# Optimization experiments

Hardware: AMD Instinct MI355X
Metric: run time of the kernel (lower is better)

Reference implementation:

```python
import jax, jax.numpy as jnp
import numpy as np

N, E, D, L = 50000, 625000, 128, 7
EPS = 1e-7   # GENConv message epsilon
T = 1.0      # softmax aggregation temperature (learn_t=False)
NUM_ATOM_FEATS, ATOM_VOCAB = 9, 64
NUM_BOND_FEATS, BOND_VOCAB = 3, 8


def setup_inputs() -> dict:
    key = jax.random.key(0)
    ks = jax.random.split(key, 9)
    x = jax.random.randint(ks[0], (N, NUM_ATOM_FEATS), 0, ATOM_VOCAB, dtype=jnp.int32)
    edge_index = jax.random.randint(ks[1], (2, E), 0, N, dtype=jnp.int32)
    edge_attr = jax.random.randint(ks[2], (E, NUM_BOND_FEATS), 0, BOND_VOCAB, dtype=jnp.int32)
    atom_emb = jax.random.normal(ks[3], (NUM_ATOM_FEATS, ATOM_VOCAB, D), dtype=jnp.float32) * 0.1
    bond_emb = jax.random.normal(ks[4], (NUM_BOND_FEATS, BOND_VOCAB, D), dtype=jnp.float32) * 0.1
    W = jax.random.normal(ks[5], (L, D, D), dtype=jnp.float32) / np.sqrt(D).astype(np.float32)
    b = jnp.zeros((L, D), dtype=jnp.float32)
    ln_gamma = jnp.ones((L, D), dtype=jnp.float32)
    ln_beta = jnp.zeros((L, D), dtype=jnp.float32)
    return dict(x=x, edge_index=edge_index, edge_attr=edge_attr,
                atom_emb=atom_emb, bond_emb=bond_emb, W=W, b=b,
                ln_gamma=ln_gamma, ln_beta=ln_beta)


def _layer_norm(h, g, bta):
    mu = jnp.mean(h, axis=-1, keepdims=True)
    var = jnp.var(h, axis=-1, keepdims=True)
    return (h - mu) * jax.lax.rsqrt(var + 1e-5) * g + bta


def _gen_conv(h, src, dst, edge_emb, Wl, bl):
    # GENConv: msg = relu(x_j + e) + eps; softmax aggregation over dst; Linear(x + m)
    msg = jax.nn.relu(h[src] + edge_emb) + EPS                 # [E, D]
    logits = msg * T
    seg_max = jax.ops.segment_max(logits, dst, num_segments=N)  # [N, D]
    seg_max = jnp.where(jnp.isfinite(seg_max), seg_max, 0.0)    # empty segments
    e = jnp.exp(logits - seg_max[dst])                          # [E, D]
    denom = jax.ops.segment_sum(e, dst, num_segments=N)         # [N, D]
    alpha = e / (denom[dst] + 1e-16)
    m = jax.ops.segment_sum(alpha * msg, dst, num_segments=N)   # [N, D]
    return (h + m) @ Wl + bl


def reference(x, edge_index, edge_attr, atom_emb, bond_emb, W, b, ln_gamma, ln_beta):
    src, dst = edge_index[0], edge_index[1]
    # AtomEncoder: sum of per-feature embedding lookups -> [N, D]
    h = jnp.sum(atom_emb[jnp.arange(NUM_ATOM_FEATS)[None, :], x], axis=1)
    # BondEncoder (conv_encode_edge=False: encoded once) -> [E, D]
    edge_emb = jnp.sum(bond_emb[jnp.arange(NUM_BOND_FEATS)[None, :], edge_attr], axis=1)
    # res+ block, dropout=0 (no-op)
    h = _gen_conv(h, src, dst, edge_emb, W[0], b[0])
    for layer in range(1, L):
        h2 = jax.nn.relu(_layer_norm(h, ln_gamma[layer - 1], ln_beta[layer - 1]))
        h = _gen_conv(h2, src, dst, edge_emb, W[layer], b[layer]) + h
    h = _layer_norm(h, ln_gamma[L - 1], ln_beta[L - 1])
    return h
```

## Files before the change

### kernel.cpp

```cpp
#include <hip/hip_runtime.h>
#include <hip/hip_fp16.h>
#include <math.h>


constexpr int D = 128;
constexpr int NA = 9;
constexpr int NB = 3;
constexpr float L2E = 1.4426950408889634f;
constexpr float INV_L2E = 0.6931471805599453f;

using half8  = __attribute__((ext_vector_type(8))) _Float16;
using h2v    = __attribute__((ext_vector_type(2))) _Float16;
using floatx4 = __attribute__((ext_vector_type(4))) float;


__global__ void k_hist(const int* __restrict__ dst, int* __restrict__ deg, int E) {
    int e = blockIdx.x * 256 + threadIdx.x;
    if (e < E) atomicAdd(&deg[dst[e]], 1);
}

__global__ void k_scan_a(const int* __restrict__ deg, int* __restrict__ offs,
                         int* __restrict__ bsum, int N) {
    __shared__ int s[256];
    int i = blockIdx.x * 256 + threadIdx.x;
    int v = (i < N) ? deg[i] : 0;
    s[threadIdx.x] = v;
    __syncthreads();
    for (int d = 1; d < 256; d <<= 1) {
        int add = (threadIdx.x >= d) ? s[threadIdx.x - d] : 0;
        __syncthreads();
        s[threadIdx.x] += add;
        __syncthreads();
    }
    if (i < N) offs[i + 1] = s[threadIdx.x];
    if (threadIdx.x == 255) bsum[blockIdx.x] = s[255];
    if (i == 0) offs[0] = 0;
}

__global__ void k_scan_b(const int* __restrict__ bsum, int* __restrict__ bexc, int nb) {
    __shared__ int s[256];
    int t = threadIdx.x;
    int v = (t < nb) ? bsum[t] : 0;
    s[t] = v;
    __syncthreads();
    for (int d = 1; d < 256; d <<= 1) {
        int add = (t >= d) ? s[t - d] : 0;
        __syncthreads();
        s[t] += add;
        __syncthreads();
    }
    if (t < nb) bexc[t] = s[t] - v;
}

__global__ void k_scan_c_dhist(int* __restrict__ offs, const int* __restrict__ bexc,
                               const int* __restrict__ deg, int* __restrict__ dbin,
                               int N) {
    __shared__ int lb[64];
    int t = threadIdx.x;
    if (t < 64) lb[t] = 0;
    __syncthreads();
    int i = blockIdx.x * 256 + t;
    if (i < N) {
        offs[i + 1] += bexc[blockIdx.x];
        int d = deg[i]; d = d < 63 ? d : 63;
        atomicAdd(&lb[63 - d], 1);
    }
    __syncthreads();
    if (t < 64 && lb[t] > 0) atomicAdd(&dbin[t], lb[t]);
}

__global__ void k_fill(const int* __restrict__ src, const int* __restrict__ dst,
                       const int* __restrict__ attr, const int* __restrict__ offs,
                       int* __restrict__ cur, unsigned* __restrict__ recs1,
                       const int* __restrict__ dbin, int* __restrict__ doff, int E) {
    int e = blockIdx.x * 256 + threadIdx.x;
    if (e < E) {
        int d = dst[e];
        int pos = offs[d] + atomicAdd(&cur[d], 1);
        unsigned cidx = (unsigned)(attr[e * 3] * 64 + attr[e * 3 + 1] * 8 + attr[e * 3 + 2]);
        recs1[pos] = (unsigned)src[e] | (cidx << 17);
    }
    if (blockIdx.x == 0 && threadIdx.x == 0) {
        int acc = 0;
        for (int b = 0; b < 64; ++b) { doff[b] = acc; acc += dbin[b]; }
    }
}


__global__ void k_dfill(const int* __restrict__ deg, const int* __restrict__ doff,
                        int* __restrict__ dcur, const int* __restrict__ offs,
                        int4* __restrict__ meta, int N) {
    __shared__ int lc[64], lbase[64];
    int t = threadIdx.x;
    if (t < 64) lc[t] = 0;
    __syncthreads();
    int i = blockIdx.x * 256 + t;
    int b = 0, rank = 0;
    if (i < N) {
        int d = deg[i]; d = d < 63 ? d : 63;
        b = 63 - d;
        rank = atomicAdd(&lc[b], 1);
    }
    __syncthreads();
    if (t < 64 && lc[t] > 0) lbase[t] = atomicAdd(&dcur[t], lc[t]);
    __syncthreads();
    if (i < N)
        meta[doff[b] + lbase[b] + rank] = make_int4(offs[i], offs[i + 1], i, 0);
}

__global__ void k_comb(const float* __restrict__ bemb, __half* __restrict__ comb16,
                       int* __restrict__ deg, int* __restrict__ cur,
                       int* __restrict__ dbin, int* __restrict__ dcur,
                       int4* __restrict__ meta, int N, int N4) {
    int gid = blockIdx.x * 256 + threadIdx.x;
    if (gid < N) { deg[gid] = 0; cur[gid] = 0; }
    if (gid < 64) { dbin[gid] = 0; dcur[gid] = 0; }
    if (gid >= N && gid < N4) meta[gid] = make_int4(0, 0, -1, 0);
    if (gid >= 512 * 32) return;
    int c = gid >> 5, q = gid & 31;
    int a0 = c >> 6, a1 = (c >> 3) & 7, a2 = c & 7;
    float4 v0 = *(const float4*)(bemb + (a0)*D + q * 4);
    float4 v1 = *(const float4*)(bemb + (8 + a1) * D + q * 4);
    float4 v2 = *(const float4*)(bemb + (16 + a2) * D + q * 4);
    __half2* c2 = (__half2*)comb16;
    c2[c * 64 + q * 2]     = __floats2half2_rn(L2E * (v0.x + v1.x + v2.x),
                                               L2E * (v0.y + v1.y + v2.y));
    c2[c * 64 + q * 2 + 1] = __floats2half2_rn(L2E * (v0.z + v1.z + v2.z),
                                               L2E * (v0.w + v1.w + v2.w));
}

__global__ void k_wt(const float* __restrict__ W, __half* __restrict__ Wt16, int total) {
    int o = blockIdx.x * 256 + threadIdx.x;
    if (o >= total) return;
    int l = o >> 14;
    int rem = o & 16383;
    int f = rem >> 7, k = rem & 127;
    Wt16[o] = __float2half_rn(W[(l << 14) + k * 128 + f]);
}


__global__ void k_atom(const int* __restrict__ x, const float* __restrict__ aemb,
                       __half* __restrict__ h16, int N) {
    int wid = (blockIdx.x * blockDim.x + threadIdx.x) >> 6;
    int lane = threadIdx.x & 63;
    if (wid >= N) return;
    const int* xr = x + wid * NA;
    float ax = 0.f, ay = 0.f;
#pragma unroll
    for (int f = 0; f < NA; ++f) {
        int v = xr[f];
        const float2 e = *(const float2*)(aemb + (f * 64 + v) * D + 2 * lane);
        ax += e.x; ay += e.y;
    }
    ((__half2*)h16)[wid * 64 + lane] = __floats2half2_rn(ax * L2E, ay * L2E);
}


__global__ __launch_bounds__(256) void k_agg(const __half* __restrict__ h16,
                      const unsigned* __restrict__ recs1,
                      const int4* __restrict__ meta,
                      const __half* __restrict__ comb16,
                      __half* __restrict__ t16, int N) {
    int w = (blockIdx.x * blockDim.x + threadIdx.x) >> 6;
    int lane = threadIdx.x & 63;
    int base = w * 4;
    if (base >= N) return;

    const h2v* hrow = (const h2v*)h16 + lane;
    const h2v* crow = (const h2v*)comb16 + lane;
    const h2v zero2 = (h2v)(_Float16)0;

    int4 m0 = meta[base], m1 = meta[base + 1], m2 = meta[base + 2], m3 = meta[base + 3];
    int su0 = __builtin_amdgcn_readfirstlane(m0.x), eu0 = __builtin_amdgcn_readfirstlane(m0.y), nid0 = __builtin_amdgcn_readfirstlane(m0.z);
    int su1 = __builtin_amdgcn_readfirstlane(m1.x), eu1 = __builtin_amdgcn_readfirstlane(m1.y), nid1 = __builtin_amdgcn_readfirstlane(m1.z);
    int su2 = __builtin_amdgcn_readfirstlane(m2.x), eu2 = __builtin_amdgcn_readfirstlane(m2.y), nid2 = __builtin_amdgcn_readfirstlane(m2.z);
    int su3 = __builtin_amdgcn_readfirstlane(m3.x), eu3 = __builtin_amdgcn_readfirstlane(m3.y), nid3 = __builtin_amdgcn_readfirstlane(m3.z);

    unsigned rv0 = 0, rv1 = 0, rv2 = 0, rv3 = 0;
    if (su0 < eu0) { int ri = su0 + lane; ri = (ri < eu0 - 1) ? ri : eu0 - 1; rv0 = recs1[ri]; }
    if (su1 < eu1) { int ri = su1 + lane; ri = (ri < eu1 - 1) ? ri : eu1 - 1; rv1 = recs1[ri]; }
    if (su2 < eu2) { int ri = su2 + lane; ri = (ri < eu2 - 1) ? ri : eu2 - 1; rv2 = recs1[ri]; }
    if (su3 < eu3) { int ri = su3 + lane; ri = (ri < eu3 - 1) ? ri : eu3 - 1; rv3 = recs1[ri]; }

    auto process = [&](int su, int eu, int nid, unsigned recv) {
        if (nid < 0) return;
        h2v hm2 = hrow[nid * 64];
        if (su >= eu) {
            ((__half2*)t16)[nid * 64 + lane] = __floats2half2_rn(
                (float)hm2[0] * INV_L2E, (float)hm2[1] * INV_L2E);
            return;
        }
        float Sx = 0.f, Sy = 0.f, Wx = 0.f, Wy = 0.f;
        h2v hq[16], cq[16];
        int e0 = su;
        bool first = true;
        do {
            int lastc = (eu < e0 + 64) ? eu : e0 + 64;
            int last = lastc - 1;
            if (!first) {
                int ri = e0 + lane;
                ri = (ri < eu - 1) ? ri : eu - 1;
                recv = recs1[ri];
            }
            first = false;

            auto load4 = [&](int b2, int slot) {
#pragma unroll
                for (int i = 0; i < 4; ++i) {
                    int idx = b2 + i; idx = (idx < last) ? idx : last;
                    unsigned r = __builtin_amdgcn_readlane(recv, idx - e0);
                    int sj = (int)(r & 0x1FFFFu);
                    int cj = (int)(r >> 17);
                    hq[slot * 4 + i] = hrow[sj * 64];
                    cq[slot * 4 + i] = crow[cj * 64];
                }
            };
            auto comp4u = [&](int slot) {
#pragma unroll
                for (int i = 0; i < 4; ++i) {
                    h2v m = hq[slot * 4 + i] + cq[slot * 4 + i];
                    m = __builtin_elementwise_max(m, zero2);
                    float u0 = (float)m[0], u1 = (float)m[1];
                    float px = __builtin_amdgcn_exp2f(u0);
                    float py = __builtin_amdgcn_exp2f(u1);
                    Sx += px; Sy += py;
                    Wx = fmaf(px, u0, Wx);
                    Wy = fmaf(py, u1, Wy);
                }
            };
            auto comp4m = [&](int gb, int slot) {
#pragma unroll
                for (int i = 0; i < 4; ++i) {
                    h2v m = hq[slot * 4 + i] + cq[slot * 4 + i];
                    m = __builtin_elementwise_max(m, zero2);
                    float u0 = (float)m[0], u1 = (float)m[1];
                    bool valid = (gb + i) < eu;
                    float px = valid ? __builtin_amdgcn_exp2f(u0) : 0.f;
                    float py = valid ? __builtin_amdgcn_exp2f(u1) : 0.f;
                    Sx += px; Sy += py;
                    Wx = fmaf(px, u0, Wx);
                    Wy = fmaf(py, u1, Wy);
                }
            };

            load4(e0, 0);
            if (e0 + 4  < lastc) load4(e0 + 4, 1);
            if (e0 + 8  < lastc) load4(e0 + 8, 2);
            if (e0 + 12 < lastc) load4(e0 + 12, 3);

            int e = e0;
            for (; e + 16 < lastc; e += 16) {
                comp4u(0); load4(e + 16, 0);
                comp4u(1); load4(e + 20, 1);
                comp4u(2); load4(e + 24, 2);
                comp4u(3); load4(e + 28, 3);
            }
            comp4m(e, 0);
            if (e + 4  < lastc) comp4m(e + 4, 1);
            if (e + 8  < lastc) comp4m(e + 8, 2);
            if (e + 12 < lastc) comp4m(e + 12, 3);

            e0 = lastc;
        } while (e0 < eu);

        float tx = ((float)hm2[0] + Wx / (Sx + 1e-16f)) * INV_L2E;
        float ty = ((float)hm2[1] + Wy / (Sy + 1e-16f)) * INV_L2E;
        ((__half2*)t16)[nid * 64 + lane] = __floats2half2_rn(tx, ty);
    };

    process(su0, eu0, nid0, rv0);
    process(su1, eu1, nid1, rv1);
    process(su2, eu2, nid2, rv2);
    process(su3, eu3, nid3, rv3);
}


template <int MODE>
__global__ __launch_bounds__(256) void k_gemm(const __half* __restrict__ A16,
                                              const __half* __restrict__ Wt16,
                                              const float* __restrict__ bl,
                                              const __half* __restrict__ res16,
                                              __half* __restrict__ hres16,
                                              const float* __restrict__ g,
                                              const float* __restrict__ bta,
                                              __half* __restrict__ h16,
                                              float* __restrict__ out,
                                              int N, int useRes) {
    __shared__ float2 sm[2][2][16];
    int lane = threadIdx.x & 63;
    int wave = threadIdx.x >> 6;
    int grp = wave >> 1, half = wave & 1;
    int quad = lane >> 4, col = lane & 15;
    int node = blockIdx.x * 32 + grp * 16 + col;
    bool nok = node < N;
    int nc = nok ? node : N - 1;

    const __half* arow = A16 + (size_t)nc * 128;
    half8 bfrag[4];
#pragma unroll
    for (int ks = 0; ks < 4; ++ks)
        bfrag[ks] = *(const half8*)(arow + ks * 32 + quad * 8);

    uint2 rr[4];
    if (useRes) {
#pragma unroll
        for (int ft2 = 0; ft2 < 4; ++ft2) {
            int f0 = (half * 4 + ft2) * 16 + quad * 4;
            rr[ft2] = *(const uint2*)(res16 + (size_t)nc * 128 + f0);
        }
    }

    floatx4 acc[4];
#pragma unroll
    for (int ft2 = 0; ft2 < 4; ++ft2) acc[ft2] = (floatx4){0.f, 0.f, 0.f, 0.f};

#pragma unroll
    for (int ft2 = 0; ft2 < 4; ++ft2) {
        const __half* wrow = Wt16 + (size_t)((half * 4 + ft2) * 16 + col) * 128;
#pragma unroll
        for (int ks = 0; ks < 4; ++ks) {
            half8 afrag = *(const half8*)(wrow + ks * 32 + quad * 8);
            acc[ft2] = __builtin_amdgcn_mfma_f32_16x16x32_f16(afrag, bfrag[ks],
                                                              acc[ft2], 0, 0, 0);
        }
    }

    float s = 0.f, ss = 0.f;
#pragma unroll
    for (int ft2 = 0; ft2 < 4; ++ft2) {
        int f0 = (half * 4 + ft2) * 16 + quad * 4;
        float4 bb = *(const float4*)(bl + f0);
        float o0 = acc[ft2][0] + bb.x, o1 = acc[ft2][1] + bb.y;
        float o2 = acc[ft2][2] + bb.z, o3 = acc[ft2][3] + bb.w;
        if (useRes) {
            __half2 r01 = *(__half2*)&rr[ft2].x, r23 = *(__half2*)&rr[ft2].y;
            o0 += __low2float(r01); o1 += __high2float(r01);
            o2 += __low2float(r23); o3 += __high2float(r23);
        }
        acc[ft2][0] = o0; acc[ft2][1] = o1; acc[ft2][2] = o2; acc[ft2][3] = o3;
        s += (o0 + o1) + (o2 + o3);
        ss += fmaf(o0, o0, o1 * o1) + fmaf(o2, o2, o3 * o3);
        if (MODE == 0 && nok) {
            __half2 h01 = __floats2half2_rn(o0, o1);
            __half2 h23 = __floats2half2_rn(o2, o3);
            uint2 pk = make_uint2(*(unsigned*)&h01, *(unsigned*)&h23);
            *(uint2*)(hres16 + (size_t)node * 128 + f0) = pk;
        }
    }
    s += __shfl_xor(s, 16, 64);  ss += __shfl_xor(ss, 16, 64);
    s += __shfl_xor(s, 32, 64);  ss += __shfl_xor(ss, 32, 64);
    if (quad == 0) sm[grp][half][col] = make_float2(s, ss);
    __syncthreads();
    float2 oth = sm[grp][half ^ 1][col];
    float st = s + oth.x, sst = ss + oth.y;
    float mu = st * (1.f / 128.f);
    float var = sst * (1.f / 128.f) - mu * mu;
    float rs = rsqrtf(var + 1e-5f);

#pragma unroll
    for (int ft2 = 0; ft2 < 4; ++ft2) {
        int f0 = (half * 4 + ft2) * 16 + quad * 4;
        float4 gg = *(const float4*)(g + f0);
        float4 bt = *(const float4*)(bta + f0);
        float l0 = (acc[ft2][0] - mu) * rs * gg.x + bt.x;
        float l1 = (acc[ft2][1] - mu) * rs * gg.y + bt.y;
        float l2 = (acc[ft2][2] - mu) * rs * gg.z + bt.z;
        float l3 = (acc[ft2][3] - mu) * rs * gg.w + bt.w;
        if (MODE == 0) {
            l0 = fmaxf(l0, 0.f); l1 = fmaxf(l1, 0.f);
            l2 = fmaxf(l2, 0.f); l3 = fmaxf(l3, 0.f);
            if (nok) {
                __half2 h01 = __floats2half2_rn(l0 * L2E, l1 * L2E);
                __half2 h23 = __floats2half2_rn(l2 * L2E, l3 * L2E);
                uint2 pk = make_uint2(*(unsigned*)&h01, *(unsigned*)&h23);
                *(uint2*)(h16 + (size_t)node * 128 + f0) = pk;
            }
        } else {
            if (nok)
                *(float4*)(out + (size_t)node * 128 + f0) =
                    make_float4(l0, l1, l2, l3);
        }
    }
}


extern "C" void kernel_launch(void* const* d_in, const int* in_sizes, int n_in,
                              void* d_out, int out_size, void* d_ws, size_t ws_size,
                              hipStream_t stream) {
    const int*   x    = (const int*)d_in[0];
    const int*   ei   = (const int*)d_in[1];
    const int*   attr = (const int*)d_in[2];
    const float* aemb = (const float*)d_in[3];
    const float* bemb = (const float*)d_in[4];
    const float* Wf   = (const float*)d_in[5];
    const float* bf   = (const float*)d_in[6];
    const float* gam  = (const float*)d_in[7];
    const float* bet  = (const float*)d_in[8];
    float* out = (float*)d_out;

    const int N = in_sizes[0] / NA;
    const int E = in_sizes[1] / 2;
    const int L = in_sizes[5] / (D * D);
    const int N4 = (N + 3) & ~3;

    char* ws = (char*)d_ws;
    size_t o = 0;
    auto carve = [&](size_t bytes) -> void* {
        void* p = (void*)(ws + o);
        o += (bytes + 255) & ~(size_t)255;
        return p;
    };
    __half* hres16 = (__half*)carve((size_t)N * D * 2);
    __half* h16    = (__half*)carve((size_t)N * D * 2);
    __half* t16    = (__half*)carve((size_t)N * D * 2);
    unsigned* recs1 = (unsigned*)carve((size_t)E * 4);
    __half* comb16 = (__half*)carve(512 * D * 2);
    __half* Wt16   = (__half*)carve((size_t)L * D * D * 2);
    int*    deg    = (int*)carve((size_t)N * 4);
    int*    cur    = (int*)carve((size_t)N * 4);
    int*    offs   = (int*)carve((size_t)(N + 1) * 4);
    int4*   meta   = (int4*)carve((size_t)N4 * 16);
    int*    dbin   = (int*)carve(256);
    int*    doff   = (int*)carve(256);
    int*    dcur   = (int*)carve(256);
    int*    bsum   = (int*)carve(4096);
    int*    bexc   = (int*)carve(4096);

    const int* src = ei;
    const int* dst = ei + E;

    int ebl = (E + 255) / 256;
    int nbl = (N + 255) / 256;

    k_comb<<<nbl, 256, 0, stream>>>(bemb, comb16, deg, cur, dbin, dcur, meta, N, N4);
    int wtot = L * D * D;
    k_wt<<<(wtot + 255) / 256, 256, 0, stream>>>(Wf, Wt16, wtot);
    k_hist<<<ebl, 256, 0, stream>>>(dst, deg, E);
    k_scan_a<<<nbl, 256, 0, stream>>>(deg, offs, bsum, N);
    k_scan_b<<<1, 256, 0, stream>>>(bsum, bexc, nbl);
    k_scan_c_dhist<<<nbl, 256, 0, stream>>>(offs, bexc, deg, dbin, N);
    k_fill<<<ebl, 256, 0, stream>>>(src, dst, attr, offs, cur, recs1, dbin, doff, E);
    k_dfill<<<nbl, 256, 0, stream>>>(deg, doff, dcur, offs, meta, N);

    int wbl = (N * 64 + 255) / 256;
    k_atom<<<wbl, 256, 0, stream>>>(x, aemb, h16, N);

    int nwv = N4 / 4;
    int abl = (nwv * 64 + 255) / 256;
    int gbl = (N + 31) / 32;
    for (int l = 0; l < L; ++l) {
        k_agg<<<abl, 256, 0, stream>>>(h16, recs1, meta, comb16, t16, N);
        if (l == L - 1) {
            k_gemm<1><<<gbl, 256, 0, stream>>>(t16, Wt16 + l * D * D, bf + l * D,
                                               hres16, hres16,
                                               gam + l * D, bet + l * D, h16, out,
                                               N, 1);
        } else {
            k_gemm<0><<<gbl, 256, 0, stream>>>(t16, Wt16 + l * D * D, bf + l * D,
                                               hres16, hres16,
                                               gam + l * D, bet + l * D, h16, out,
                                               N, l > 0 ? 1 : 0);
        }
    }
}
```

Measured before the change: 590.2 us.

## Fuse setup kernels, drop cursor array, pad edge records to remove clamps

Merges the bond-combination, weight-transpose and zeroing kernels into one setup kernel, and merges the degree-bucket fill with the atom encoder, cutting the launch count. The fill step now advances the offsets array in place with atomics, which removes the separate cursor array. Start and end offsets are then read from the shifted offsets. The edge record buffer is padded with 64 zeroed entries so the aggregation kernel can drop index clamping when it loads records. Chunks shrink from 64 to 48 edges, likely so that readlane indices stay within the wavefront after the clamp is removed.

```diff
diff --git a/kernel.cpp b/kernel.cpp
--- a/kernel.cpp
+++ b/kernel.cpp
@@ -12,6 +12,37 @@
 using half8  = __attribute__((ext_vector_type(8))) _Float16;
 using h2v    = __attribute__((ext_vector_type(2))) _Float16;
 using floatx4 = __attribute__((ext_vector_type(4))) float;
+
+
+__global__ void k_setup0(const float* __restrict__ bemb, __half* __restrict__ comb16,
+                         const float* __restrict__ W, __half* __restrict__ Wt16,
+                         int* __restrict__ deg, int* __restrict__ dbin,
+                         int* __restrict__ dcur, int4* __restrict__ meta,
+                         unsigned* __restrict__ recs1,
+                         int N, int N4, int wtot, int E) {
+    int gid = blockIdx.x * 256 + threadIdx.x;
+    if (gid < N) deg[gid] = 0;
+    if (gid < 64) { dbin[gid] = 0; dcur[gid] = 0; recs1[E + gid] = 0; }
+    if (gid >= N && gid < N4) meta[gid] = make_int4(0, 0, -1, 0);
+    if (gid < 512 * 32) {
+        int c = gid >> 5, q = gid & 31;
+        int a0 = c >> 6, a1 = (c >> 3) & 7, a2 = c & 7;
+        float4 v0 = *(const float4*)(bemb + (a0)*D + q * 4);
+        float4 v1 = *(const float4*)(bemb + (8 + a1) * D + q * 4);
+        float4 v2 = *(const float4*)(bemb + (16 + a2) * D + q * 4);
+        __half2* c2 = (__half2*)comb16;
+        c2[c * 64 + q * 2]     = __floats2half2_rn(L2E * (v0.x + v1.x + v2.x),
+                                                   L2E * (v0.y + v1.y + v2.y));
+        c2[c * 64 + q * 2 + 1] = __floats2half2_rn(L2E * (v0.z + v1.z + v2.z),
+                                                   L2E * (v0.w + v1.w + v2.w));
+    }
+    if (gid < wtot) {
+        int l = gid >> 14;
+        int rem = gid & 16383;
+        int f = rem >> 7, k = rem & 127;
+        Wt16[gid] = __float2half_rn(W[(l << 14) + k * 128 + f]);
+    }
+}
 
 
 __global__ void k_hist(const int* __restrict__ dst, int* __restrict__ deg, int E) {
@@ -70,13 +101,13 @@
 }
 
 __global__ void k_fill(const int* __restrict__ src, const int* __restrict__ dst,
-                       const int* __restrict__ attr, const int* __restrict__ offs,
-                       int* __restrict__ cur, unsigned* __restrict__ recs1,
+                       const int* __restrict__ attr, int* __restrict__ offs,
+                       unsigned* __restrict__ recs1,
                        const int* __restrict__ dbin, int* __restrict__ doff, int E) {
     int e = blockIdx.x * 256 + threadIdx.x;
     if (e < E) {
         int d = dst[e];
-        int pos = offs[d] + atomicAdd(&cur[d], 1);
+        int pos = atomicAdd(&offs[d], 1);
         unsigned cidx = (unsigned)(attr[e * 3] * 64 + attr[e * 3 + 1] * 8 + attr[e * 3 + 2]);
         recs1[pos] = (unsigned)src[e] | (cidx << 17);
     }
@@ -87,60 +118,32 @@
 }
 
 
-__global__ void k_dfill(const int* __restrict__ deg, const int* __restrict__ doff,
-                        int* __restrict__ dcur, const int* __restrict__ offs,
-                        int4* __restrict__ meta, int N) {
-    __shared__ int lc[64], lbase[64];
-    int t = threadIdx.x;
-    if (t < 64) lc[t] = 0;
-    __syncthreads();
-    int i = blockIdx.x * 256 + t;
-    int b = 0, rank = 0;
-    if (i < N) {
-        int d = deg[i]; d = d < 63 ? d : 63;
-        b = 63 - d;
-        rank = atomicAdd(&lc[b], 1);
-    }
-    __syncthreads();
-    if (t < 64 && lc[t] > 0) lbase[t] = atomicAdd(&dcur[t], lc[t]);
-    __syncthreads();
-    if (i < N)
-        meta[doff[b] + lbase[b] + rank] = make_int4(offs[i], offs[i + 1], i, 0);
-}
-
-__global__ void k_comb(const float* __restrict__ bemb, __half* __restrict__ comb16,
-                       int* __restrict__ deg, int* __restrict__ cur,
-                       int* __restrict__ dbin, int* __restrict__ dcur,
-                       int4* __restrict__ meta, int N, int N4) {
-    int gid = blockIdx.x * 256 + threadIdx.x;
-    if (gid < N) { deg[gid] = 0; cur[gid] = 0; }
-    if (gid < 64) { dbin[gid] = 0; dcur[gid] = 0; }
-    if (gid >= N && gid < N4) meta[gid] = make_int4(0, 0, -1, 0);
-    if (gid >= 512 * 32) return;
-    int c = gid >> 5, q = gid & 31;
-    int a0 = c >> 6, a1 = (c >> 3) & 7, a2 = c & 7;
-    float4 v0 = *(const float4*)(bemb + (a0)*D + q * 4);
-    float4 v1 = *(const float4*)(bemb + (8 + a1) * D + q * 4);
-    float4 v2 = *(const float4*)(bemb + (16 + a2) * D + q * 4);
-    __half2* c2 = (__half2*)comb16;
-    c2[c * 64 + q * 2]     = __floats2half2_rn(L2E * (v0.x + v1.x + v2.x),
-                                               L2E * (v0.y + v1.y + v2.y));
-    c2[c * 64 + q * 2 + 1] = __floats2half2_rn(L2E * (v0.z + v1.z + v2.z),
-                                               L2E * (v0.w + v1.w + v2.w));
-}
-
-__global__ void k_wt(const float* __restrict__ W, __half* __restrict__ Wt16, int total) {
-    int o = blockIdx.x * 256 + threadIdx.x;
-    if (o >= total) return;
-    int l = o >> 14;
-    int rem = o & 16383;
-    int f = rem >> 7, k = rem & 127;
-    Wt16[o] = __float2half_rn(W[(l << 14) + k * 128 + f]);
-}
-
-
-__global__ void k_atom(const int* __restrict__ x, const float* __restrict__ aemb,
-                       __half* __restrict__ h16, int N) {
+__global__ void k_dfill_atom(const int* __restrict__ deg, const int* __restrict__ doff,
+                             int* __restrict__ dcur, const int* __restrict__ offs,
+                             int4* __restrict__ meta,
+                             const int* __restrict__ x, const float* __restrict__ aemb,
+                             __half* __restrict__ h16, int N, int nbl) {
+    if ((int)blockIdx.x < nbl) {
+        __shared__ int lc[64], lbase[64];
+        int t = threadIdx.x;
+        if (t < 64) lc[t] = 0;
+        __syncthreads();
+        int i = blockIdx.x * 256 + t;
+        int b = 0, rank = 0;
+        if (i < N) {
+            int d = deg[i]; d = d < 63 ? d : 63;
+            b = 63 - d;
+            rank = atomicAdd(&lc[b], 1);
+        }
+        __syncthreads();
+        if (t < 64 && lc[t] > 0) lbase[t] = atomicAdd(&dcur[t], lc[t]);
+        __syncthreads();
+        if (i < N) {
+            int su = (i > 0) ? offs[i - 1] : 0;
+            int eu = offs[i];
+            meta[doff[b] + lbase[b] + rank] = make_int4(su, eu, i, 0);
+        }
+    }
     int wid = (blockIdx.x * blockDim.x + threadIdx.x) >> 6;
     int lane = threadIdx.x & 63;
     if (wid >= N) return;
@@ -177,10 +180,10 @@
     int su3 = __builtin_amdgcn_readfirstlane(m3.x), eu3 = __builtin_amdgcn_readfirstlane(m3.y), nid3 = __builtin_amdgcn_readfirstlane(m3.z);
 
     unsigned rv0 = 0, rv1 = 0, rv2 = 0, rv3 = 0;
-    if (su0 < eu0) { int ri = su0 + lane; ri = (ri < eu0 - 1) ? ri : eu0 - 1; rv0 = recs1[ri]; }
-    if (su1 < eu1) { int ri = su1 + lane; ri = (ri < eu1 - 1) ? ri : eu1 - 1; rv1 = recs1[ri]; }
-    if (su2 < eu2) { int ri = su2 + lane; ri = (ri < eu2 - 1) ? ri : eu2 - 1; rv2 = recs1[ri]; }
-    if (su3 < eu3) { int ri = su3 + lane; ri = (ri < eu3 - 1) ? ri : eu3 - 1; rv3 = recs1[ri]; }
+    if (su0 < eu0) rv0 = recs1[su0 + lane];
+    if (su1 < eu1) rv1 = recs1[su1 + lane];
+    if (su2 < eu2) rv2 = recs1[su2 + lane];
+    if (su3 < eu3) rv3 = recs1[su3 + lane];
 
     auto process = [&](int su, int eu, int nid, unsigned recv) {
         if (nid < 0) return;
@@ -193,22 +196,13 @@
         float Sx = 0.f, Sy = 0.f, Wx = 0.f, Wy = 0.f;
         h2v hq[16], cq[16];
         int e0 = su;
-        bool first = true;
-        do {
-            int lastc = (eu < e0 + 64) ? eu : e0 + 64;
-            int last = lastc - 1;
-            if (!first) {
-                int ri = e0 + lane;
-                ri = (ri < eu - 1) ? ri : eu - 1;
-                recv = recs1[ri];
-            }
-            first = false;
+        for (;;) {
+            int lastc = (eu < e0 + 48) ? eu : e0 + 48;
 
             auto load4 = [&](int b2, int slot) {
 #pragma unroll
                 for (int i = 0; i < 4; ++i) {
-                    int idx = b2 + i; idx = (idx < last) ? idx : last;
-                    unsigned r = __builtin_amdgcn_readlane(recv, idx - e0);
+                    unsigned r = __builtin_amdgcn_readlane(recv, b2 + i - e0);
                     int sj = (int)(r & 0x1FFFFu);
                     int cj = (int)(r >> 17);
                     hq[slot * 4 + i] = hrow[sj * 64];
@@ -234,7 +228,7 @@
                     h2v m = hq[slot * 4 + i] + cq[slot * 4 + i];
                     m = __builtin_elementwise_max(m, zero2);
                     float u0 = (float)m[0], u1 = (float)m[1];
-                    bool valid = (gb + i) < eu;
+                    bool valid = (gb + i) < lastc;
                     float px = valid ? __builtin_amdgcn_exp2f(u0) : 0.f;
                     float py = valid ? __builtin_amdgcn_exp2f(u1) : 0.f;
                     Sx += px; Sy += py;
@@ -261,7 +255,9 @@
             if (e + 12 < lastc) comp4m(e + 12, 3);
 
             e0 = lastc;
-        } while (e0 < eu);
+            if (e0 >= eu) break;
+            recv = recs1[e0 + lane];
+        }
 
         float tx = ((float)hm2[0] + Wx / (Sx + 1e-16f)) * INV_L2E;
         float ty = ((float)hm2[1] + Wy / (Sy + 1e-16f)) * INV_L2E;
@@ -413,11 +409,10 @@
     __half* hres16 = (__half*)carve((size_t)N * D * 2);
     __half* h16    = (__half*)carve((size_t)N * D * 2);
     __half* t16    = (__half*)carve((size_t)N * D * 2);
-    unsigned* recs1 = (unsigned*)carve((size_t)E * 4);
+    unsigned* recs1 = (unsigned*)carve((size_t)(E + 64) * 4);
     __half* comb16 = (__half*)carve(512 * D * 2);
     __half* Wt16   = (__half*)carve((size_t)L * D * D * 2);
     int*    deg    = (int*)carve((size_t)N * 4);
-    int*    cur    = (int*)carve((size_t)N * 4);
     int*    offs   = (int*)carve((size_t)(N + 1) * 4);
     int4*   meta   = (int4*)carve((size_t)N4 * 16);
     int*    dbin   = (int*)carve(256);
@@ -431,19 +426,21 @@
 
     int ebl = (E + 255) / 256;
     int nbl = (N + 255) / 256;
-
-    k_comb<<<nbl, 256, 0, stream>>>(bemb, comb16, deg, cur, dbin, dcur, meta, N, N4);
     int wtot = L * D * D;
-    k_wt<<<(wtot + 255) / 256, 256, 0, stream>>>(Wf, Wt16, wtot);
+    int s0max = wtot > N4 ? wtot : N4;
+    int sbl = (s0max + 255) / 256;
+
+    k_setup0<<<sbl, 256, 0, stream>>>(bemb, comb16, Wf, Wt16, deg, dbin, dcur,
+                                      meta, recs1, N, N4, wtot, E);
     k_hist<<<ebl, 256, 0, stream>>>(dst, deg, E);
     k_scan_a<<<nbl, 256, 0, stream>>>(deg, offs, bsum, N);
     k_scan_b<<<1, 256, 0, stream>>>(bsum, bexc, nbl);
     k_scan_c_dhist<<<nbl, 256, 0, stream>>>(offs, bexc, deg, dbin, N);
-    k_fill<<<ebl, 256, 0, stream>>>(src, dst, attr, offs, cur, recs1, dbin, doff, E);
-    k_dfill<<<nbl, 256, 0, stream>>>(deg, doff, dcur, offs, meta, N);
+    k_fill<<<ebl, 256, 0, stream>>>(src, dst, attr, offs, recs1, dbin, doff, E);
 
     int wbl = (N * 64 + 255) / 256;
-    k_atom<<<wbl, 256, 0, stream>>>(x, aemb, h16, N);
+    k_dfill_atom<<<wbl, 256, 0, stream>>>(deg, doff, dcur, offs, meta,
+                                          x, aemb, h16, N, nbl);
 
     int nwv = N4 / 4;
     int abl = (nwv * 64 + 255) / 256;
```

Measured after the change: 589.4 us. No clear change (-0.1%).
